# Kernel optimization log

Hardware: AMD Instinct MI355X
Metric: run time of the kernel (lower is better)

## Reference

```python
import jax, jax.numpy as jnp
import numpy as np

N_HEAD = 16
COND_LEN = 256  # n_unmasked; mask[i, j] == 1 iff j < COND_LEN + i


def rotate_half(x):
    # interleaved pairs: (x0, x1, x2, x3, ...) -> (-x1, x0, -x3, x2, ...)
    x = x.reshape(x.shape[:-1] + (-1, 2))
    x1, x2 = x[..., 0], x[..., 1]
    return jnp.stack([-x2, x1], axis=-1).reshape(x.shape[:-2] + (-1,))


def apply_rotary_pos_emb(t, freqs):
    # t: [B, H, T, l], freqs: [T, l] -> broadcast over B, H
    return t * jnp.cos(freqs) + rotate_half(t) * jnp.sin(freqs)


def setup_inputs() -> dict:
    key = jax.random.key(0)
    ks = jax.random.split(key, 12)
    B, T, C = 8, 769, 1024
    l = 32
    s = 0.02
    return {
        "x_q": jax.random.normal(ks[0], (B, T, C), jnp.float32),
        "x_kv": jax.random.normal(ks[1], (B, T, C), jnp.float32),
        "rotary_pos_emb": jax.random.uniform(ks[2], (T, l), jnp.float32),
        "Wq": jax.random.normal(ks[3], (C, C), jnp.float32) * s,
        "bq": jnp.zeros((C,), jnp.float32),
        "Wk": jax.random.normal(ks[4], (C, C), jnp.float32) * s,
        "bk": jnp.zeros((C,), jnp.float32),
        "Wv": jax.random.normal(ks[5], (C, C), jnp.float32) * s,
        "bv": jnp.zeros((C,), jnp.float32),
        "Wp": jax.random.normal(ks[6], (C, C), jnp.float32) * s,
        "bp": jnp.zeros((C,), jnp.float32),
    }


def reference(x_q, x_kv, rotary_pos_emb, Wq, bq, Wk, bk, Wv, bv, Wp, bp):
    B, T_q, C = x_q.shape
    T_kv = x_kv.shape[1]
    H = N_HEAD
    hd = C // H

    def heads(x, W, b, T):
        return (x @ W.T + b).reshape(B, T, H, hd).transpose(0, 2, 1, 3)  # [B,H,T,hd]

    q = heads(x_q, Wq, bq, T_q)
    k = heads(x_kv, Wk, bk, T_kv)
    v = heads(x_kv, Wv, bv, T_kv)

    # partial rotary on first l dims of q and k
    l = rotary_pos_emb.shape[-1]
    q = jnp.concatenate([apply_rotary_pos_emb(q[..., :l], rotary_pos_emb), q[..., l:]], axis=-1)
    k = jnp.concatenate([apply_rotary_pos_emb(k[..., :l], rotary_pos_emb), k[..., l:]], axis=-1)

    att = jnp.einsum("bhqd,bhkd->bhqk", q, k) * (1.0 / jnp.sqrt(jnp.asarray(hd, q.dtype)))
    # custom prefix+causal mask: allowed iff col < COND_LEN + row
    row = jnp.arange(T_q)[:, None]
    col = jnp.arange(T_kv)[None, :]
    allowed = col < (COND_LEN + row)  # [T_q, T_kv]
    att = jnp.where(allowed[None, None], att, -jnp.inf)
    att = jax.nn.softmax(att, axis=-1)

    y = jnp.einsum("bhqk,bhkd->bhqd", att, v)
    y = y.transpose(0, 2, 1, 3).reshape(B, T_q, C)
    return y @ Wp.T + bp
```

## Files before the change

kernel.cpp:

```cpp
#include <hip/hip_runtime.h>
#include <stdint.h>

#define B_    8
#define T_    769
#define C_    1024
#define H_    16
#define COND_ 256
#define NTOK  (B_*T_)
#define BH_   (B_*H_)
#define TP_   896

typedef short    v8s  __attribute__((ext_vector_type(8)));
typedef float    v4f  __attribute__((ext_vector_type(4)));
typedef uint16_t u16x4 __attribute__((ext_vector_type(4)));
typedef uint16_t u16x8 __attribute__((ext_vector_type(8)));

__device__ __forceinline__ uint16_t f2bf(float f) {
  uint32_t u = __builtin_bit_cast(uint32_t, f);
  u += 0x7fffu + ((u >> 16) & 1u);
  return (uint16_t)(u >> 16);
}
__device__ __forceinline__ float bf2f(uint16_t h) {
  uint32_t u = ((uint32_t)h) << 16;
  return __builtin_bit_cast(float, u);
}

__device__ __forceinline__ void gl_lds16(const void* gptr, void* lptr) {
  __builtin_amdgcn_global_load_lds(
      (const __attribute__((address_space(1))) uint32_t*)gptr,
      (__attribute__((address_space(3))) uint32_t*)lptr,
      16, 0, 0);
}

__global__ __launch_bounds__(256) void convert_bf16(
    const float* xq, const float* xkv, const float* wq, const float* wk,
    const float* wv, const float* wp,
    uint16_t* dxq, uint16_t* dxkv, uint16_t* dwq, uint16_t* dwk,
    uint16_t* dwv, uint16_t* dwp)
{
  int bid = blockIdx.x;
  const float* s; uint16_t* d; int base;
  if (bid < 6152)       { s = xq;  d = dxq;  base = bid; }
  else if (bid < 12304) { s = xkv; d = dxkv; base = bid - 6152; }
  else {
    int r = bid - 12304;
    int wsel = r >> 10; base = r & 1023;
    s = (wsel == 0) ? wq : (wsel == 1) ? wk : (wsel == 2) ? wv : wp;
    d = (wsel == 0) ? dwq : (wsel == 1) ? dwk : (wsel == 2) ? dwv : dwp;
  }
  int i = base * 256 + threadIdx.x;
  float4 f = ((const float4*)s)[i];
  u16x4 o;
  o[0] = f2bf(f.x); o[1] = f2bf(f.y); o[2] = f2bf(f.z); o[3] = f2bf(f.w);
  ((u16x4*)d)[i] = o;
}

__device__ __forceinline__ void gemm_mainloop64(
    const uint16_t* A, const uint16_t* W, int M, int row0, int col0,
    v4f acc[4][4], uint16_t* sA, uint16_t* sB)
{
  const int tid = threadIdx.x;
  const int lane = tid & 63, w = tid >> 6, quad = lane >> 4, l15 = lane & 15;
  const int rbase = (w >> 1) * 64, cbase = (w & 1) * 64;

  const uint16_t* Aptr[4];
  const uint16_t* Bptr[4];
  #pragma unroll
  for (int r = 0; r < 4; r++) {
    int c = r * 256 + tid;
    int row = c >> 3, qp = c & 7;
    int g = qp ^ (row & 7);
    Aptr[r] = A + (size_t)min(row0 + row, M - 1) * 1024 + g * 8;
    Bptr[r] = W + (size_t)(col0 + row) * 1024 + g * 8;
  }

  #pragma unroll
  for (int i = 0; i < 4; i++)
    #pragma unroll
    for (int j = 0; j < 4; j++) acc[i][j] = (v4f)0.0f;

  for (int k0 = 0; k0 < 1024; k0 += 64) {
    #pragma unroll
    for (int r = 0; r < 4; r++) {
      gl_lds16(Aptr[r] + k0, sA + (r * 256 + tid) * 8);
      gl_lds16(Bptr[r] + k0, sB + (r * 256 + tid) * 8);
    }
    __syncthreads();
    #pragma unroll
    for (int s = 0; s < 2; s++) {
      v8s af[4], bf[4];
      #pragma unroll
      for (int i = 0; i < 4; i++) {
        int m = rbase + i * 16 + l15;
        af[i] = *(const v8s*)(sA + m * 64 + (((s * 4 + quad) ^ (m & 7)) * 8));
      }
      #pragma unroll
      for (int j = 0; j < 4; j++) {
        int n = cbase + j * 16 + l15;
        bf[j] = *(const v8s*)(sB + n * 64 + (((s * 4 + quad) ^ (n & 7)) * 8));
      }
      #pragma unroll
      for (int i = 0; i < 4; i++)
        #pragma unroll
        for (int j = 0; j < 4; j++)
          acc[i][j] = __builtin_amdgcn_mfma_f32_16x16x32_bf16(af[i], bf[j], acc[i][j], 0, 0, 0);
    }
    __syncthreads();
  }
}

__global__ __launch_bounds__(256) void gemm_qkv(
    const uint16_t* xq, const uint16_t* xkv, const uint16_t* Wqkv,
    const float* bq, const float* bk, const float* bv, const float* freqs,
    uint16_t* Q, uint16_t* K, uint16_t* V)
{
  __shared__ uint16_t sA[128 * 64];
  __shared__ uint16_t sB[128 * 64];
  const int ct = blockIdx.x, rt = blockIdx.y;
  const int z = ct >> 3;
  const int col0 = ct * 128, row0 = rt * 128;
  const uint16_t* A = (z == 0) ? xq : xkv;
  const float* bias  = (z == 0) ? bq : (z == 1 ? bk : bv);
  uint16_t* dst      = (z == 0) ? Q  : (z == 1 ? K  : V);

  v4f acc[4][4];
  gemm_mainloop64(A, Wqkv, NTOK, row0, col0, acc, sA, sB);

  const int tid = threadIdx.x;
  const int lane = tid & 63, w = tid >> 6, quad = lane >> 4, l15 = lane & 15;
  const int rbase = (w >> 1) * 64, cbase = (w & 1) * 64;
  #pragma unroll
  for (int i = 0; i < 4; i++) {
    #pragma unroll
    for (int reg = 0; reg < 4; reg++) {
      int n = row0 + rbase + i * 16 + quad * 4 + reg;
      bool ok = (n < NTOK);
      int nn = min(n, NTOK - 1);
      int b = nn / T_, t = nn % T_;
      float vj[4];
      #pragma unroll
      for (int j = 0; j < 4; j++)
        vj[j] = acc[i][j][reg] + bias[(col0 + cbase + j * 16 + l15) & 1023];
      if (z < 2) {
        float v0 = vj[0], v1 = vj[1];
        float p0 = __shfl_xor(v0, 1);
        float p1 = __shfl_xor(v1, 1);
        float f0 = freqs[t * 32 + l15];
        float f1 = freqs[t * 32 + 16 + l15];
        float s0, c0, s1, c1;
        __sincosf(f0, &s0, &c0);
        __sincosf(f1, &s1, &c1);
        if (l15 & 1) { vj[0] = v0 * c0 + p0 * s0; vj[1] = v1 * c1 + p1 * s1; }
        else         { vj[0] = v0 * c0 - p0 * s0; vj[1] = v1 * c1 - p1 * s1; }
      }
      if (z == 0) {
        #pragma unroll
        for (int j = 0; j < 4; j++) vj[j] *= 0.125f;
      }
      if (ok) {
        #pragma unroll
        for (int j = 0; j < 4; j++) {
          int col = col0 + cbase + j * 16 + l15;
          int h = (col >> 6) & 15, d = col & 63;
          dst[((size_t)(b * H_ + h) * T_ + t) * 64 + d] = f2bf(vj[j]);
        }
      }
    }
  }
}

__global__ __launch_bounds__(256) void gemm_out(
    const uint16_t* Y, const uint16_t* wp, const float* bp, float* out)
{
  __shared__ uint16_t sA[128 * 64];
  __shared__ uint16_t sB[128 * 64];
  const int col0 = blockIdx.x * 128, row0 = blockIdx.y * 128;
  v4f acc[4][4];
  gemm_mainloop64(Y, wp, NTOK, row0, col0, acc, sA, sB);

  const int tid = threadIdx.x;
  const int lane = tid & 63, w = tid >> 6, quad = lane >> 4, l15 = lane & 15;
  const int rbase = (w >> 1) * 64, cbase = (w & 1) * 64;
  #pragma unroll
  for (int i = 0; i < 4; i++) {
    #pragma unroll
    for (int reg = 0; reg < 4; reg++) {
      int n = row0 + rbase + i * 16 + quad * 4 + reg;
      if (n < NTOK) {
        #pragma unroll
        for (int j = 0; j < 4; j++) {
          int col = col0 + cbase + j * 16 + l15;
          out[(size_t)n * 1024 + col] = acc[i][j][reg] + bp[col];
        }
      }
    }
  }
}

__global__ __launch_bounds__(256) void transpose_v(const uint16_t* Vb, uint16_t* Vt)
{
  __shared__ uint16_t sT[64 * 64];
  const int tid = threadIdx.x;
  const int t0 = blockIdx.x * 64, bh = blockIdx.y;
  const uint16_t* src = Vb + (size_t)bh * T_ * 64;
  #pragma unroll
  for (int r = 0; r < 2; r++) {
    int task = r * 256 + tid;
    int t = task >> 3, oc = task & 7;
    int gt = min(t0 + t, T_ - 1);
    u16x8 v = *(const u16x8*)(src + (size_t)gt * 64 + oc * 8);
    int p = oc ^ (t & 7) ^ ((t >> 3) & 7);
    *(u16x8*)(sT + t * 64 + p * 8) = v;
  }
  __syncthreads();
  uint16_t* dst = Vt + (size_t)bh * 64 * TP_;
  #pragma unroll
  for (int r = 0; r < 2; r++) {
    int task = r * 256 + tid;
    int o = task & 7, d = task >> 3;
    u16x8 v;
    #pragma unroll
    for (int k = 0; k < 8; k++) {
      int t = o * 8 + k;
      int p = (d >> 3) ^ k ^ o;
      v[k] = sT[t * 64 + p * 8 + (d & 7)];
    }
    *(u16x8*)(dst + (size_t)d * TP_ + t0 + o * 8) = v;
  }
}

__global__ __launch_bounds__(256) void attn(
    const uint16_t* Q, const uint16_t* K, const uint16_t* Vt, uint16_t* Y)
{
  __shared__ uint16_t sK[128 * 64];
  __shared__ uint16_t sVT[64 * 128];
  __shared__ uint16_t sP[4 * 16 * 136];

  const int tid = threadIdx.x;
  const int lane = tid & 63, w = tid >> 6, quad = lane >> 4, l15 = lane & 15;
  const int bh = blockIdx.y, b = bh >> 4, h = bh & 15;
  const int q0 = blockIdx.x * 64;

  const uint16_t* Qb = Q + (size_t)bh * T_ * 64;
  const uint16_t* Kb = K + (size_t)bh * T_ * 64;
  const uint16_t* Vtb = Vt + (size_t)bh * 64 * TP_;

  const int qr = min(q0 + w * 16 + l15, T_ - 1);
  v8s aq0 = *(const v8s*)(Qb + (size_t)qr * 64 + quad * 8);
  v8s aq1 = *(const v8s*)(Qb + (size_t)qr * 64 + 32 + quad * 8);

  float l_r[4] = {0.f, 0.f, 0.f, 0.f};
  v4f o[4];
  #pragma unroll
  for (int r = 0; r < 4; r++) o[r] = (v4f)0.0f;

  const int kend = min(T_, q0 + 319);
  const int nkt = (kend + 127) >> 7;

  for (int kt = 0; kt < nkt; kt++) {
    const int k0 = kt * 128;
    #pragma unroll
    for (int r = 0; r < 4; r++) {
      int c = r * 256 + tid;
      int key = c >> 3, qp = c & 7;
      int g = qp ^ (key & 7);
      int gk = min(k0 + key, T_ - 1);
      gl_lds16(Kb + (size_t)gk * 64 + g * 8, sK + c * 8);
    }
    #pragma unroll
    for (int r = 0; r < 4; r++) {
      int c = r * 256 + tid;
      int d = c >> 4, p = c & 15;
      int g = (p & 8) | ((p ^ d) & 7);
      gl_lds16(Vtb + (size_t)d * TP_ + k0 + g * 8, sVT + c * 8);
    }
    __syncthreads();

    v4f s[8];
    #pragma unroll
    for (int cb = 0; cb < 8; cb++) {
      int key_l = cb * 16 + l15;
      v8s b0 = *(const v8s*)(sK + (key_l * 8 + ((quad) ^ (key_l & 7))) * 8);
      v8s b1 = *(const v8s*)(sK + (key_l * 8 + ((4 + quad) ^ (key_l & 7))) * 8);
      v4f zz = (v4f)0.0f;
      zz = __builtin_amdgcn_mfma_f32_16x16x32_bf16(aq0, b0, zz, 0, 0, 0);
      zz = __builtin_amdgcn_mfma_f32_16x16x32_bf16(aq1, b1, zz, 0, 0, 0);
      s[cb] = zz;
    }

    uint16_t* pw = sP + w * (16 * 136);
    const int qrow_base = q0 + w * 16 + quad * 4;
    const bool full = (k0 + 128 <= COND_ + q0) && (k0 + 128 <= T_);
    if (full) {
      #pragma unroll
      for (int reg = 0; reg < 4; reg++) {
        float rs = 0.f;
        #pragma unroll
        for (int cb = 0; cb < 8; cb++) {
          float pv = __expf(s[cb][reg]);
          uint16_t pb = f2bf(pv);
          rs += bf2f(pb);
          pw[(quad * 4 + reg) * 136 + cb * 16 + l15] = pb;
        }
        #pragma unroll
        for (int off = 1; off < 16; off <<= 1) rs += __shfl_xor(rs, off);
        l_r[reg] += rs;
      }
    } else {
      #pragma unroll
      for (int reg = 0; reg < 4; reg++) {
        int lim = min(COND_ + qrow_base + reg, T_);
        float rs = 0.f;
        #pragma unroll
        for (int cb = 0; cb < 8; cb++) {
          int key = k0 + cb * 16 + l15;
          float pv = (key < lim) ? __expf(s[cb][reg]) : 0.f;
          uint16_t pb = f2bf(pv);
          rs += bf2f(pb);
          pw[(quad * 4 + reg) * 136 + cb * 16 + l15] = pb;
        }
        #pragma unroll
        for (int off = 1; off < 16; off <<= 1) rs += __shfl_xor(rs, off);
        l_r[reg] += rs;
      }
    }

    #pragma unroll
    for (int ks = 0; ks < 4; ks++) {
      v8s ap = *(const v8s*)(pw + l15 * 136 + ks * 32 + quad * 8);
      #pragma unroll
      for (int cbd = 0; cbd < 4; cbd++) {
        int d = cbd * 16 + l15;
        v8s bv = *(const v8s*)(sVT + d * 128 + (((ks * 4 + quad) ^ (d & 7)) * 8));
        o[cbd] = __builtin_amdgcn_mfma_f32_16x16x32_bf16(ap, bv, o[cbd], 0, 0, 0);
      }
    }
    __syncthreads();
  }

  #pragma unroll
  for (int reg = 0; reg < 4; reg++) {
    int t = q0 + w * 16 + quad * 4 + reg;
    if (t < T_) {
      float inv = 1.0f / l_r[reg];
      #pragma unroll
      for (int cbd = 0; cbd < 4; cbd++) {
        int d = cbd * 16 + l15;
        Y[((size_t)(b * T_ + t)) * C_ + h * 64 + d] = f2bf(o[cbd][reg] * inv);
      }
    }
  }
}

extern "C" void kernel_launch(void* const* d_in, const int* in_sizes, int n_in,
                              void* d_out, int out_size, void* d_ws, size_t ws_size,
                              hipStream_t stream)
{
  const float* x_q   = (const float*)d_in[0];
  const float* x_kv  = (const float*)d_in[1];
  const float* freqs = (const float*)d_in[2];
  const float* Wq = (const float*)d_in[3];
  const float* bq = (const float*)d_in[4];
  const float* Wk = (const float*)d_in[5];
  const float* bk = (const float*)d_in[6];
  const float* Wv = (const float*)d_in[7];
  const float* bv = (const float*)d_in[8];
  const float* Wp = (const float*)d_in[9];
  const float* bp = (const float*)d_in[10];
  float* out = (float*)d_out;

  const size_t SZX = (size_t)NTOK * C_;
  const size_t SZW = (size_t)C_ * C_;
  uint16_t* ws = (uint16_t*)d_ws;
  uint16_t* xq_bf  = ws;
  uint16_t* xkv_bf = xq_bf + SZX;
  uint16_t* wq_bf  = xkv_bf + SZX;
  uint16_t* wk_bf  = wq_bf + SZW;
  uint16_t* wv_bf  = wk_bf + SZW;
  uint16_t* wp_bf  = wv_bf + SZW;
  uint16_t* Qb = wp_bf + SZW;
  uint16_t* Kb = Qb + SZX;
  uint16_t* Vb = Kb + SZX;
  uint16_t* Vt = ws;
  uint16_t* Yb = Vb;

  convert_bf16<<<dim3(16400), 256, 0, stream>>>(
      x_q, x_kv, Wq, Wk, Wv, Wp, xq_bf, xkv_bf, wq_bf, wk_bf, wv_bf, wp_bf);

  gemm_qkv<<<dim3(24, 49), 256, 0, stream>>>(
      xq_bf, xkv_bf, wq_bf, bq, bk, bv, freqs, Qb, Kb, Vb);

  transpose_v<<<dim3(13, BH_), 256, 0, stream>>>(Vb, Vt);

  attn<<<dim3(13, BH_), 256, 0, stream>>>(Qb, Kb, Vt, Yb);

  gemm_out<<<dim3(8, 49), 256, 0, stream>>>(Yb, wp_bf, bp, out);
}
```

Baseline: 278.0 us.

## Double-buffer LDS tiles in GEMM mainloop to overlap loads with MFMA

Converts the projection GEMM mainloop into a two-stage ping-pong pipeline: the next K-slice is issued via global-to-LDS loads into a second buffer while MFMAs consume the current one, with one barrier per stage. LDS per block doubles to 64 KB, which may reduce blocks resident per CU. The aim is to hide global memory latency in the QKV and output projection GEMMs.

```diff
diff --git a/kernel.cpp b/kernel.cpp
--- a/kernel.cpp
+++ b/kernel.cpp
@@ -55,6 +55,43 @@
   ((u16x4*)d)[i] = o;
 }
 
+
+__device__ __forceinline__ void gemm_stage64(
+    const uint16_t* const Aptr[4], const uint16_t* const Bptr[4],
+    int k0, uint16_t* sA, uint16_t* sB, int tid)
+{
+  #pragma unroll
+  for (int r = 0; r < 4; r++) {
+    gl_lds16(Aptr[r] + k0, sA + (r * 256 + tid) * 8);
+    gl_lds16(Bptr[r] + k0, sB + (r * 256 + tid) * 8);
+  }
+}
+
+__device__ __forceinline__ void gemm_compute64(
+    const uint16_t* sAc, const uint16_t* sBc, v4f acc[4][4],
+    int rbase, int cbase, int quad, int l15)
+{
+  #pragma unroll
+  for (int s = 0; s < 2; s++) {
+    v8s af[4], bfv[4];
+    #pragma unroll
+    for (int i = 0; i < 4; i++) {
+      int m = rbase + i * 16 + l15;
+      af[i] = *(const v8s*)(sAc + m * 64 + (((s * 4 + quad) ^ (m & 7)) * 8));
+    }
+    #pragma unroll
+    for (int j = 0; j < 4; j++) {
+      int n = cbase + j * 16 + l15;
+      bfv[j] = *(const v8s*)(sBc + n * 64 + (((s * 4 + quad) ^ (n & 7)) * 8));
+    }
+    #pragma unroll
+    for (int i = 0; i < 4; i++)
+      #pragma unroll
+      for (int j = 0; j < 4; j++)
+        acc[i][j] = __builtin_amdgcn_mfma_f32_16x16x32_bf16(af[i], bfv[j], acc[i][j], 0, 0, 0);
+  }
+}
+
 __device__ __forceinline__ void gemm_mainloop64(
     const uint16_t* A, const uint16_t* W, int M, int row0, int col0,
     v4f acc[4][4], uint16_t* sA, uint16_t* sB)
@@ -79,32 +116,20 @@
     #pragma unroll
     for (int j = 0; j < 4; j++) acc[i][j] = (v4f)0.0f;
 
-  for (int k0 = 0; k0 < 1024; k0 += 64) {
-    #pragma unroll
-    for (int r = 0; r < 4; r++) {
-      gl_lds16(Aptr[r] + k0, sA + (r * 256 + tid) * 8);
-      gl_lds16(Bptr[r] + k0, sB + (r * 256 + tid) * 8);
-    }
+  uint16_t* sA0 = sA;         uint16_t* sB0 = sB;
+  uint16_t* sA1 = sA + 8192;  uint16_t* sB1 = sB + 8192;
+
+  gemm_stage64(Aptr, Bptr, 0, sA0, sB0, tid);
+  __syncthreads();
+
+  #pragma unroll 1
+  for (int t = 0; t < 16; t += 2) {
+    gemm_stage64(Aptr, Bptr, (t + 1) * 64, sA1, sB1, tid);
+    gemm_compute64(sA0, sB0, acc, rbase, cbase, quad, l15);
     __syncthreads();
-    #pragma unroll
-    for (int s = 0; s < 2; s++) {
-      v8s af[4], bf[4];
-      #pragma unroll
-      for (int i = 0; i < 4; i++) {
-        int m = rbase + i * 16 + l15;
-        af[i] = *(const v8s*)(sA + m * 64 + (((s * 4 + quad) ^ (m & 7)) * 8));
-      }
-      #pragma unroll
-      for (int j = 0; j < 4; j++) {
-        int n = cbase + j * 16 + l15;
-        bf[j] = *(const v8s*)(sB + n * 64 + (((s * 4 + quad) ^ (n & 7)) * 8));
-      }
-      #pragma unroll
-      for (int i = 0; i < 4; i++)
-        #pragma unroll
-        for (int j = 0; j < 4; j++)
-          acc[i][j] = __builtin_amdgcn_mfma_f32_16x16x32_bf16(af[i], bf[j], acc[i][j], 0, 0, 0);
-    }
+    if (t + 2 < 16)
+      gemm_stage64(Aptr, Bptr, (t + 2) * 64, sA0, sB0, tid);
+    gemm_compute64(sA1, sB1, acc, rbase, cbase, quad, l15);
     __syncthreads();
   }
 }
@@ -114,8 +139,8 @@
     const float* bq, const float* bk, const float* bv, const float* freqs,
     uint16_t* Q, uint16_t* K, uint16_t* V)
 {
-  __shared__ uint16_t sA[128 * 64];
-  __shared__ uint16_t sB[128 * 64];
+  __shared__ uint16_t sA[2 * 128 * 64];
+  __shared__ uint16_t sB[2 * 128 * 64];
   const int ct = blockIdx.x, rt = blockIdx.y;
   const int z = ct >> 3;
   const int col0 = ct * 128, row0 = rt * 128;
@@ -172,8 +197,8 @@
 __global__ __launch_bounds__(256) void gemm_out(
     const uint16_t* Y, const uint16_t* wp, const float* bp, float* out)
 {
-  __shared__ uint16_t sA[128 * 64];
-  __shared__ uint16_t sB[128 * 64];
+  __shared__ uint16_t sA[2 * 128 * 64];
+  __shared__ uint16_t sB[2 * 128 * 64];
   const int col0 = blockIdx.x * 128, row0 = blockIdx.y * 128;
   v4f acc[4][4];
   gemm_mainloop64(Y, wp, NTOK, row0, col0, acc, sA, sB);
```

Result: no change. 283.3 us (+1.9%).
